# Kernel optimization log

Measured on AMD Instinct MI355X. Metric: run time of the kernel, lower is better.

The kernel has to match this reference:

```python
import jax, jax.numpy as jnp
import numpy as np

N, M, FIN, FOUT, E = 8, 50000, 32, 32, 800000


def setup_inputs() -> dict:
    key = jax.random.key(0)
    ks = jax.random.split(key, 6)
    x = jax.random.normal(ks[0], (N, M, FIN), dtype=jnp.float32)
    adj_rows = jax.random.randint(ks[1], (E,), 0, M, dtype=jnp.int32)
    adj_cols = jax.random.randint(ks[2], (E,), 0, M, dtype=jnp.int32)
    adj_vals = jax.random.uniform(ks[3], (E,), dtype=jnp.float32)
    stdv = 1.0 / np.sqrt(FOUT)
    weight = jax.random.uniform(ks[4], (FIN, FOUT), dtype=jnp.float32, minval=-stdv, maxval=stdv)
    bias = jax.random.uniform(ks[5], (FOUT,), dtype=jnp.float32, minval=-stdv, maxval=stdv)
    return {"x": x, "adj_rows": adj_rows, "adj_cols": adj_cols,
            "adj_vals": adj_vals, "weight": weight, "bias": bias}


def reference(x, adj_rows, adj_cols, adj_vals, weight, bias):
    # spmm(adj, x) over the node axis M for every batch element.
    # adj is COO: out[:, r, :] += v * x[:, c, :] for each edge (r, c, v).
    xe = jnp.take(x, adj_cols, axis=1) * adj_vals[None, :, None]  # [N, E, Fin]
    y = jnp.zeros_like(x).at[:, adj_rows, :].add(xe)              # [N, M, Fin]
    # dense linear + bias: (N*M, Fin) @ (Fin, Fout) + bias
    return jnp.einsum('nmf,fo->nmo', y, weight) + bias
```

## Files before the change

kernel.cpp:

```cpp
#include <hip/hip_runtime.h>
#include <hip/hip_bf16.h>

#define NB 8
#define MN 50000
#define FI 32
#define FO 32
#define NE 800000
#define CAPLOG 6
#define CAP 64
#define BINSHIFT 7
#define BINROWS 128
#define NBINS 391
#define BINCAPLOG 12
#define BIN_BLOCKS 392

typedef float        f32x4 __attribute__((ext_vector_type(4)));
typedef unsigned int u32x4 __attribute__((ext_vector_type(4)));

__global__ __launch_bounds__(256) void gemm_xw(const float* __restrict__ x,
                                               const float* __restrict__ W,
                                               unsigned int* __restrict__ zb,
                                               int* __restrict__ gCursor) {
    int bid = blockIdx.x;
    int t   = threadIdx.x;

    if (bid == 0) {
        for (int i = t; i < NBINS; i += 256) gCursor[i] = i << BINCAPLOG;
    }

    __shared__ float Ws[FI * FO];
    ((float4*)Ws)[t] = ((const float4*)W)[t];
    __syncthreads();

    int n     = bid / 3125;
    int mb    = bid % 3125;
    int rowid = t >> 4;
    int j     = t & 15;
    int m     = mb * 16 + rowid;

    const float4* xr = (const float4*)(x + ((long)n * MN + m) * FI);
    float4 xv[8];
#pragma unroll
    for (int i = 0; i < 8; ++i) xv[i] = xr[i];
    const float* xf = (const float*)xv;

    float a0 = 0.f, a1 = 0.f;
#pragma unroll
    for (int k = 0; k < FI; ++k) {
        a0 += xf[k] * Ws[k * FO + 2 * j];
        a1 += xf[k] * Ws[k * FO + 2 * j + 1];
    }
    unsigned int lo = (unsigned int)__bfloat16_as_ushort(__float2bfloat16(a0));
    unsigned int hi = (unsigned int)__bfloat16_as_ushort(__float2bfloat16(a1));
    zb[(long)m * 128 + n * 16 + j] = lo | (hi << 16);
}

__global__ __launch_bounds__(256) void bin_edges(const int* __restrict__ rows,
                                                 const int* __restrict__ cols,
                                                 const float* __restrict__ vals,
                                                 int* __restrict__ gCursor,
                                                 unsigned long long* __restrict__ sorted) {
    __shared__ int cnt[NBINS];
    __shared__ int base[NBINS];
    int t = threadIdx.x;
    for (int i = t; i < NBINS; i += 256) cnt[i] = 0;
    __syncthreads();

    unsigned long long pk[8];
    int bn[8], rk[8];
    int e0 = blockIdx.x * 2048;
#pragma unroll
    for (int k = 0; k < 8; ++k) {
        int e = e0 + k * 256 + t;
        bn[k] = -1;
        if (e < NE) {
            int r = rows[e];
            unsigned int vb = (unsigned int)__bfloat16_as_ushort(__float2bfloat16(vals[e]));
            pk[k] = ((unsigned long long)(unsigned int)r << 32) |
                    (unsigned long long)((vb << 16) | (unsigned int)cols[e]);
            bn[k] = r >> BINSHIFT;
            rk[k] = atomicAdd(&cnt[bn[k]], 1);
        }
    }
    __syncthreads();
    for (int i = t; i < NBINS; i += 256) base[i] = atomicAdd(&gCursor[i], cnt[i]);
    __syncthreads();
#pragma unroll
    for (int k = 0; k < 8; ++k) {
        if (bn[k] >= 0) {
            int pos = base[bn[k]] + rk[k];
            if (pos < ((bn[k] + 1) << BINCAPLOG))
                sorted[pos] = pk[k];
        }
    }
}

__global__ __launch_bounds__(1024) void fill_sorted(const unsigned long long* __restrict__ sorted,
                                                    const int* __restrict__ gCursor,
                                                    unsigned int* __restrict__ bucket,
                                                    int* __restrict__ cursor) {
    __shared__ int cur[BINROWS];
    int t   = threadIdx.x;
    int bin = blockIdx.x;
    if (t < BINROWS) cur[t] = 0;
    __syncthreads();

    int beg = bin << BINCAPLOG;
    int cnt = gCursor[bin] - beg;
    if (cnt > (1 << BINCAPLOG)) cnt = (1 << BINCAPLOG);

    for (int i = t; i < cnt; i += 1024) {
        unsigned long long pk = __builtin_nontemporal_load(&sorted[beg + i]);
        int r  = (int)(pk >> 32);
        int lr = r & (BINROWS - 1);
        int p  = atomicAdd(&cur[lr], 1);
        if (p < CAP)
            bucket[((long)r << CAPLOG) + p] = (unsigned int)pk;
    }
    __syncthreads();
    if (t < BINROWS) {
        int R = (bin << BINSHIFT) + t;
        if (R < MN) cursor[R] = cur[t] > CAP ? CAP : cur[t];
    }
}

__global__ __launch_bounds__(256) void aggregate(const u32x4* __restrict__ zb4,
                                                 const int* __restrict__ cursor,
                                                 const unsigned int* __restrict__ bucket,
                                                 const float* __restrict__ bias,
                                                 f32x4* __restrict__ out4) {
    int lane = threadIdx.x & 63;
    int r    = blockIdx.x * 4 + (threadIdx.x >> 6);

    int cnt = cursor[r];
    cnt = cnt > CAP ? CAP : cnt;

    unsigned int mypk = __builtin_nontemporal_load(&bucket[(r << CAPLOG) + lane]);

    int half = lane >> 5;
    int sub  = lane & 31;

    float acc[8];
#pragma unroll
    for (int k = 0; k < 8; ++k) acc[k] = 0.f;

    int i = 0;
    for (; i + 8 <= cnt; i += 8) {
        unsigned int pk[4];
        u32x4 zv[4];
#pragma unroll
        for (int k = 0; k < 4; ++k) pk[k] = __shfl(mypk, i + 2 * k + half);
#pragma unroll
        for (int k = 0; k < 4; ++k) zv[k] = zb4[((long)(pk[k] & 0xffff) << 5) + sub];
#pragma unroll
        for (int k = 0; k < 4; ++k) {
            float v = __uint_as_float(pk[k] & 0xffff0000u);
#pragma unroll
            for (int q = 0; q < 4; ++q) {
                unsigned int w = zv[k][q];
                acc[2 * q]     += v * __uint_as_float(w << 16);
                acc[2 * q + 1] += v * __uint_as_float(w & 0xffff0000u);
            }
        }
    }
    for (; i + 2 <= cnt; i += 2) {
        unsigned int pk0 = __shfl(mypk, i + half);
        u32x4 zv0 = zb4[((long)(pk0 & 0xffff) << 5) + sub];
        float v = __uint_as_float(pk0 & 0xffff0000u);
#pragma unroll
        for (int q = 0; q < 4; ++q) {
            unsigned int w = zv0[q];
            acc[2 * q]     += v * __uint_as_float(w << 16);
            acc[2 * q + 1] += v * __uint_as_float(w & 0xffff0000u);
        }
    }
    if (i < cnt) {
        unsigned int pk0 = __shfl(mypk, i);
        int   c = (half == 0) ? (int)(pk0 & 0xffff) : 0;
        float v = (half == 0) ? __uint_as_float(pk0 & 0xffff0000u) : 0.f;
        u32x4 zv0 = zb4[((long)c << 5) + sub];
#pragma unroll
        for (int q = 0; q < 4; ++q) {
            unsigned int w = zv0[q];
            acc[2 * q]     += v * __uint_as_float(w << 16);
            acc[2 * q + 1] += v * __uint_as_float(w & 0xffff0000u);
        }
    }

#pragma unroll
    for (int k = 0; k < 8; ++k) acc[k] += __shfl_xor(acc[k], 32);

    if (half == 0) {
        int n  = sub >> 2;
        int j4 = sub & 3;
        const float* bb = bias + j4 * 8;
        f32x4 o0 = {acc[0] + bb[0], acc[1] + bb[1], acc[2] + bb[2], acc[3] + bb[3]};
        f32x4 o1 = {acc[4] + bb[4], acc[5] + bb[5], acc[6] + bb[6], acc[7] + bb[7]};
        long ob = ((long)n * MN + r) * 8 + j4 * 2;
        __builtin_nontemporal_store(o0, &out4[ob]);
        __builtin_nontemporal_store(o1, &out4[ob + 1]);
    }
}

extern "C" void kernel_launch(void* const* d_in, const int* in_sizes, int n_in,
                              void* d_out, int out_size, void* d_ws, size_t ws_size,
                              hipStream_t stream) {
    const float* x    = (const float*)d_in[0];
    const int*   rows = (const int*)d_in[1];
    const int*   cols = (const int*)d_in[2];
    const float* vals = (const float*)d_in[3];
    const float* W    = (const float*)d_in[4];
    const float* bias = (const float*)d_in[5];
    f32x4* out4 = (f32x4*)d_out;

    char* ws = (char*)d_ws;
    size_t off_z      = 0;
    size_t off_cursor = off_z + (size_t)MN * NB * FO * 2;
    size_t off_gcur   = off_cursor + (size_t)MN * 4;
    size_t off_bucket = off_gcur + (((size_t)NBINS * 4 + 127) & ~(size_t)127);
    size_t off_sorted = off_bucket + (size_t)MN * CAP * 4;

    unsigned int*       zb      = (unsigned int*)(ws + off_z);
    int*                cursor  = (int*)(ws + off_cursor);
    int*                gCursor = (int*)(ws + off_gcur);
    unsigned int*       bucket  = (unsigned int*)(ws + off_bucket);
    unsigned long long* sorted  = (unsigned long long*)(ws + off_sorted);

    gemm_xw<<<25000, 256, 0, stream>>>(x, W, zb, gCursor);

    bin_edges<<<BIN_BLOCKS, 256, 0, stream>>>(rows, cols, vals, gCursor, sorted);

    fill_sorted<<<NBINS, 1024, 0, stream>>>(sorted, gCursor, bucket, cursor);

    aggregate<<<MN / 4, 256, 0, stream>>>((const u32x4*)zb, cursor, bucket, bias, out4);
}
```

Measured before the change: 119.8 us.

## Replace fixed-capacity row buckets with per-bin compacted CSR and larger binning blocks

fill_sorted now runs a per-bin prefix scan over row counts and writes edges into a compacted per-bin dense array, storing each row's packed offset and count in a single int. Previously every row used a 64-slot bucket. This shrinks the bucket footprint written and read (about 12.8 MB down to about 6.4 MB) and lets aggregate fetch offset and count with one load. bin_edges also moves to 1024-thread blocks over 8192 edges each, cutting global cursor atomics by 4x but leaving fewer blocks to fill the GPU. The scan adds several block-wide syncs to fill_sorted.

```diff
diff --git a/kernel.cpp b/kernel.cpp
--- a/kernel.cpp
+++ b/kernel.cpp
@@ -6,13 +6,12 @@
 #define FI 32
 #define FO 32
 #define NE 800000
-#define CAPLOG 6
 #define CAP 64
 #define BINSHIFT 7
 #define BINROWS 128
 #define NBINS 391
 #define BINCAPLOG 12
-#define BIN_BLOCKS 392
+#define BIN_BLOCKS 98
 
 typedef float        f32x4 __attribute__((ext_vector_type(4)));
 typedef unsigned int u32x4 __attribute__((ext_vector_type(4)));
@@ -55,23 +54,23 @@
     zb[(long)m * 128 + n * 16 + j] = lo | (hi << 16);
 }
 
-__global__ __launch_bounds__(256) void bin_edges(const int* __restrict__ rows,
-                                                 const int* __restrict__ cols,
-                                                 const float* __restrict__ vals,
-                                                 int* __restrict__ gCursor,
-                                                 unsigned long long* __restrict__ sorted) {
+__global__ __launch_bounds__(1024) void bin_edges(const int* __restrict__ rows,
+                                                  const int* __restrict__ cols,
+                                                  const float* __restrict__ vals,
+                                                  int* __restrict__ gCursor,
+                                                  unsigned long long* __restrict__ sorted) {
     __shared__ int cnt[NBINS];
     __shared__ int base[NBINS];
     int t = threadIdx.x;
-    for (int i = t; i < NBINS; i += 256) cnt[i] = 0;
+    for (int i = t; i < NBINS; i += 1024) cnt[i] = 0;
     __syncthreads();
 
     unsigned long long pk[8];
     int bn[8], rk[8];
-    int e0 = blockIdx.x * 2048;
+    int e0 = blockIdx.x * 8192;
 #pragma unroll
     for (int k = 0; k < 8; ++k) {
-        int e = e0 + k * 256 + t;
+        int e = e0 + k * 1024 + t;
         bn[k] = -1;
         if (e < NE) {
             int r = rows[e];
@@ -83,7 +82,7 @@
         }
     }
     __syncthreads();
-    for (int i = t; i < NBINS; i += 256) base[i] = atomicAdd(&gCursor[i], cnt[i]);
+    for (int i = t; i < NBINS; i += 1024) base[i] = atomicAdd(&gCursor[i], cnt[i]);
     __syncthreads();
 #pragma unroll
     for (int k = 0; k < 8; ++k) {
@@ -97,45 +96,70 @@
 
 __global__ __launch_bounds__(1024) void fill_sorted(const unsigned long long* __restrict__ sorted,
                                                     const int* __restrict__ gCursor,
-                                                    unsigned int* __restrict__ bucket,
-                                                    int* __restrict__ cursor) {
-    __shared__ int cur[BINROWS];
+                                                    unsigned int* __restrict__ dense,
+                                                    int* __restrict__ posCnt) {
+    __shared__ int cntS[BINROWS];
+    __shared__ int pfx[BINROWS];
+    __shared__ int exS[BINROWS];
     int t   = threadIdx.x;
     int bin = blockIdx.x;
-    if (t < BINROWS) cur[t] = 0;
+    if (t < BINROWS) cntS[t] = 0;
     __syncthreads();
 
     int beg = bin << BINCAPLOG;
-    int cnt = gCursor[bin] - beg;
-    if (cnt > (1 << BINCAPLOG)) cnt = (1 << BINCAPLOG);
-
-    for (int i = t; i < cnt; i += 1024) {
-        unsigned long long pk = __builtin_nontemporal_load(&sorted[beg + i]);
-        int r  = (int)(pk >> 32);
-        int lr = r & (BINROWS - 1);
-        int p  = atomicAdd(&cur[lr], 1);
-        if (p < CAP)
-            bucket[((long)r << CAPLOG) + p] = (unsigned int)pk;
-    }
-    __syncthreads();
+    int n = gCursor[bin] - beg;
+    if (n > (1 << BINCAPLOG)) n = 1 << BINCAPLOG;
+
+    unsigned long long pk[4];
+    int lr[4], sl[4];
+#pragma unroll
+    for (int k = 0; k < 4; ++k) {
+        int i = t + k * 1024;
+        lr[k] = -1;
+        if (i < n) {
+            pk[k] = __builtin_nontemporal_load(&sorted[beg + i]);
+            lr[k] = ((int)(pk[k] >> 32)) & (BINROWS - 1);
+            sl[k] = atomicAdd(&cntS[lr[k]], 1);
+        }
+    }
+    __syncthreads();
+
+    if (t < BINROWS) pfx[t] = cntS[t] > CAP ? CAP : cntS[t];
+    __syncthreads();
+    for (int off = 1; off < BINROWS; off <<= 1) {
+        int v = (t < BINROWS && t >= off) ? pfx[t - off] : 0;
+        __syncthreads();
+        if (t < BINROWS) pfx[t] += v;
+        __syncthreads();
+    }
     if (t < BINROWS) {
+        int cc = cntS[t] > CAP ? CAP : cntS[t];
+        exS[t] = pfx[t] - cc;
         int R = (bin << BINSHIFT) + t;
-        if (R < MN) cursor[R] = cur[t] > CAP ? CAP : cur[t];
+        if (R < MN) posCnt[R] = ((beg + exS[t]) << 7) | cc;
+    }
+    __syncthreads();
+
+#pragma unroll
+    for (int k = 0; k < 4; ++k) {
+        if (lr[k] >= 0 && sl[k] < CAP)
+            dense[beg + exS[lr[k]] + sl[k]] = (unsigned int)pk[k];
     }
 }
 
 __global__ __launch_bounds__(256) void aggregate(const u32x4* __restrict__ zb4,
-                                                 const int* __restrict__ cursor,
-                                                 const unsigned int* __restrict__ bucket,
+                                                 const int* __restrict__ posCnt,
+                                                 const unsigned int* __restrict__ dense,
                                                  const float* __restrict__ bias,
                                                  f32x4* __restrict__ out4) {
     int lane = threadIdx.x & 63;
     int r    = blockIdx.x * 4 + (threadIdx.x >> 6);
 
-    int cnt = cursor[r];
-    cnt = cnt > CAP ? CAP : cnt;
-
-    unsigned int mypk = __builtin_nontemporal_load(&bucket[(r << CAPLOG) + lane]);
+    int pc  = posCnt[r];
+    int cnt = pc & 127;
+    long pos = (unsigned int)pc >> 7;
+
+    unsigned int mypk = __builtin_nontemporal_load(&dense[pos + lane]);
 
     int half = lane >> 5;
     int sub  = lane & 31;
@@ -215,22 +239,22 @@
 
     char* ws = (char*)d_ws;
     size_t off_z      = 0;
-    size_t off_cursor = off_z + (size_t)MN * NB * FO * 2;
-    size_t off_gcur   = off_cursor + (size_t)MN * 4;
-    size_t off_bucket = off_gcur + (((size_t)NBINS * 4 + 127) & ~(size_t)127);
-    size_t off_sorted = off_bucket + (size_t)MN * CAP * 4;
+    size_t off_pc     = off_z + (size_t)MN * NB * FO * 2;
+    size_t off_gcur   = off_pc + (size_t)MN * 4;
+    size_t off_dense  = off_gcur + (((size_t)NBINS * 4 + 127) & ~(size_t)127);
+    size_t off_sorted = off_dense + (((size_t)NBINS << BINCAPLOG) + 64) * 4;
 
     unsigned int*       zb      = (unsigned int*)(ws + off_z);
-    int*                cursor  = (int*)(ws + off_cursor);
+    int*                posCnt  = (int*)(ws + off_pc);
     int*                gCursor = (int*)(ws + off_gcur);
-    unsigned int*       bucket  = (unsigned int*)(ws + off_bucket);
+    unsigned int*       dense   = (unsigned int*)(ws + off_dense);
     unsigned long long* sorted  = (unsigned long long*)(ws + off_sorted);
 
     gemm_xw<<<25000, 256, 0, stream>>>(x, W, zb, gCursor);
 
-    bin_edges<<<BIN_BLOCKS, 256, 0, stream>>>(rows, cols, vals, gCursor, sorted);
-
-    fill_sorted<<<NBINS, 1024, 0, stream>>>(sorted, gCursor, bucket, cursor);
-
-    aggregate<<<MN / 4, 256, 0, stream>>>((const u32x4*)zb, cursor, bucket, bias, out4);
-}
+    bin_edges<<<BIN_BLOCKS, 1024, 0, stream>>>(rows, cols, vals, gCursor, sorted);
+
+    fill_sorted<<<NBINS, 1024, 0, stream>>>(sorted, gCursor, dense, posCnt);
+
+    aggregate<<<MN / 4, 256, 0, stream>>>((const u32x4*)zb, posCnt, dense, bias, out4);
+}
```

After: 115.5 us. 1.04x faster.
